# Kernel optimization log

Hardware: AMD Instinct MI355X
Metric: run time of the kernel (lower is better)

Reference implementation:

```python
import jax, jax.numpy as jnp
import numpy as np

B, N = 8, 1000
EMB, K, F1E, F1V, MSG = 4, 3, 2, 3, 2


def cross_concat(h):
    # h: [b, n, d] -> [b, n, n, 2d], interleaving (h_i, h_j) per feature (stack axis=-1 then reshape)
    b, n, d = h.shape
    hi = jnp.broadcast_to(h[:, :, None, :], (b, n, n, d))
    hj = jnp.broadcast_to(h[:, None, :, :], (b, n, n, d))
    return jnp.stack((hi, hj), axis=-1).reshape(b, n, n, 2 * d)


def setup_inputs() -> dict:
    key = jax.random.key(0)
    ks = jax.random.split(key, 16)
    p = lambda k, s: (jax.random.normal(k, s, dtype=jnp.float32) * 0.1)
    return {
        "x": jax.random.normal(ks[0], (B, N), dtype=jnp.float32),
        "W1_emb": p(ks[1], (1, EMB)), "b1_emb": p(ks[2], (EMB,)),
        "W2_emb": p(ks[3], (1, EMB)), "b2_emb": p(ks[4], (EMB,)),
        "W_f1e": p(ks[5], (2 * EMB, F1E)), "b_f1e": p(ks[6], (F1E,)),
        "W_f2e": p(ks[7], (2 * F1V, K)), "b_f2e": p(ks[8], (K,)),
        "W_fk": p(ks[9], (K, 2 * EMB, MSG)), "b_fk": p(ks[10], (K, MSG)),
        "W_f1v": p(ks[11], (F1E, F1V)), "b_f1v": p(ks[12], (F1V,)),
        "W_f2v": p(ks[13], (MSG + 1, 1)), "b_f2v": p(ks[14], (1,)),
    }


def reference(x, W1_emb, b1_emb, W2_emb, b2_emb, W_f1e, b_f1e, W_f2e, b_f2e,
              W_fk, b_fk, W_f1v, b_f1v, W_f2v, b_f2v):
    x_ = x[..., None]                                  # [B,N,1]
    h1 = x_ @ W1_emb + b1_emb                          # [B,N,EMB]
    c = cross_concat(h1)                               # [B,N,N,2*EMB]
    h = jnp.sum(c @ W_f1e + b_f1e, axis=2)             # [B,N,F1E]
    h2 = h @ W_f1v + b_f1v                             # [B,N,F1V]
    c2 = cross_concat(h2)                              # [B,N,N,2*F1V]
    hsum = jnp.sum(c2, axis=0)                         # [N,N,2*F1V] (sum over batch)
    edge_logits = hsum @ W_f2e + b_f2e                 # [N,N,K]
    edge_probs = jax.nn.softmax(edge_logits, axis=-1)  # [N,N,K]
    h1_ = x_ @ W2_emb + b2_emb                         # [B,N,EMB]
    c3 = cross_concat(h1_)                             # [B,N,N,2*EMB]
    # K per-relation edge MLPs, stacked on the last axis -> [B,N,N,MSG,K]
    messages = jnp.einsum('bijd,kdm->bijmk', c3, W_fk) + b_fk.T
    # softmax-weighted combine, summed over receiver axis j and relation axis k
    v_e = jnp.einsum('ijk,bijmk->bim', edge_probs, messages)  # [B,N,MSG]
    h2_ = x_ + (jnp.concatenate((v_e, x_), axis=-1) @ W_f2v + b_f2v)
    return jnp.squeeze(h2_, axis=-1)                   # [B,N]
```

## Files before the change

kernel.cpp:

```cpp
#include <hip/hip_runtime.h>

#define NN 1000

__device__ __forceinline__ float wave_sum(float v) {
#pragma unroll
    for (int o = 32; o > 0; o >>= 1) v += __shfl_xor(v, o, 64);
    return v;
}

__global__ __launch_bounds__(256) void fused_kernel(
    const float* __restrict__ x,
    const float* __restrict__ W1, const float* __restrict__ b1,
    const float* __restrict__ W2, const float* __restrict__ b2,
    const float* __restrict__ Wf1e, const float* __restrict__ bf1e,
    const float* __restrict__ Wf2e, const float* __restrict__ bf2e,
    const float* __restrict__ Wfk, const float* __restrict__ bfk,
    const float* __restrict__ Wf1v, const float* __restrict__ bf1v,
    const float* __restrict__ Wf2v, const float* __restrict__ bf2v,
    float* __restrict__ out) {
    const int wave = threadIdx.x >> 6;
    const int lane = threadIdx.x & 63;
    const int i = blockIdx.x * 4 + wave;

    float4 v[4][8];
#pragma unroll
    for (int t = 0; t < 4; ++t) {
        const int j4 = lane + 64 * t;
        if (j4 < NN / 4) {
#pragma unroll
            for (int b = 0; b < 8; ++b)
                v[t][b] = *reinterpret_cast<const float4*>(x + b * NN + 4 * j4);
        }
    }

    float Xs[8];
#pragma unroll
    for (int b = 0; b < 8; ++b) {
        float sb = 0.f;
#pragma unroll
        for (int t = 0; t < 4; ++t)
            if (lane + 64 * t < NN / 4)
                sb += (v[t][b].x + v[t][b].y) + (v[t][b].z + v[t][b].w);
        Xs[b] = wave_sum(sb);
    }
    const float S = ((Xs[0] + Xs[1]) + (Xs[2] + Xs[3])) +
                    ((Xs[4] + Xs[5]) + (Xs[6] + Xs[7]));

    float alpha[2];
#pragma unroll
    for (int f = 0; f < 2; ++f) {
        float a = 0.f;
#pragma unroll
        for (int e = 0; e < 4; ++e) a += W1[e] * Wf1e[(2 * e) * 2 + f];
        alpha[f] = (float)NN * a;
    }
    float gamma[3];
#pragma unroll
    for (int vv = 0; vv < 3; ++vv) {
        float g = 0.f;
#pragma unroll
        for (int f = 0; f < 2; ++f) g += alpha[f] * Wf1v[f * 3 + vv];
        gamma[vv] = g;
    }
    float uA[6], cB[6], vAc[6];
#pragma unroll
    for (int m = 0; m < 2; ++m)
#pragma unroll
        for (int k = 0; k < 3; ++k) {
            float ua = 0.f, ub = 0.f, va = 0.f, vb = 0.f;
#pragma unroll
            for (int e = 0; e < 4; ++e) {
                float wE = Wfk[k * 16 + (2 * e) * 2 + m];
                float wO = Wfk[k * 16 + (2 * e + 1) * 2 + m];
                ua += W2[e] * wE; ub += b2[e] * wE;
                va += W2[e] * wO; vb += b2[e] * wO;
            }
            uA[m * 3 + k]  = ua;
            cB[m * 3 + k]  = ub + vb + bfk[k * 2 + m];
            vAc[m * 3 + k] = va;
        }
    float Bsum[2];
#pragma unroll
    for (int f = 0; f < 2; ++f) {
        float t0 = 0.f, t1 = 0.f;
#pragma unroll
        for (int e = 0; e < 4; ++e) {
            t0 += b1[e] * Wf1e[(2 * e) * 2 + f];
            t1 += (S * W1[e] + 8.f * (float)NN * b1[e]) * Wf1e[(2 * e + 1) * 2 + f];
        }
        Bsum[f] = 8.f * (float)NN * t0 + t1 + 8.f * (float)NN * bf1e[f];
    }
    float Ds[3];
#pragma unroll
    for (int vv = 0; vv < 3; ++vv) {
        float d = 8.f * bf1v[vv];
#pragma unroll
        for (int f = 0; f < 2; ++f) d += Bsum[f] * Wf1v[f * 3 + vv];
        Ds[vv] = d;
    }
    const float LOG2E = 1.4426950408889634f;
    float PB[3], AiQ[3];
    {
        float xsi = 0.f;
#pragma unroll
        for (int b = 0; b < 8; ++b) xsi += x[b * NN + i];
#pragma unroll
        for (int k = 0; k < 3; ++k) {
            float PA = 0.f, QA = 0.f, pb = 0.f, qb = 0.f;
#pragma unroll
            for (int vv = 0; vv < 3; ++vv) {
                PA += gamma[vv] * Wf2e[(2 * vv) * 3 + k];
                QA += Ds[vv]    * Wf2e[(2 * vv) * 3 + k];
                pb += gamma[vv] * Wf2e[(2 * vv + 1) * 3 + k];
                qb += Ds[vv]    * Wf2e[(2 * vv + 1) * 3 + k];
            }
            PB[k]  = pb * LOG2E;
            AiQ[k] = (PA * xsi + QA + bf2e[k] + qb) * LOG2E;
        }
    }

    const float ai0 = AiQ[0], ai1 = AiQ[1], ai2 = AiQ[2];
    const float pb0 = PB[0], pb1 = PB[1], pb2 = PB[2];
    float Q0 = 0.f, Q1 = 0.f;
    float R[8][2];
#pragma unroll
    for (int b = 0; b < 8; ++b) { R[b][0] = 0.f; R[b][1] = 0.f; }

#pragma unroll
    for (int t = 0; t < 4; ++t) {
        if (lane + 64 * t < NN / 4) {
            const float* vf = reinterpret_cast<const float*>(v[t]);
#pragma unroll
            for (int u = 0; u < 4; ++u) {
                float xs = 0.f;
#pragma unroll
                for (int b = 0; b < 8; ++b) xs += vf[b * 4 + u];
                float l0 = ai0 + pb0 * xs, l1 = ai1 + pb1 * xs, l2 = ai2 + pb2 * xs;
                float mx = fmaxf(l0, fmaxf(l1, l2));
                float e0 = exp2f(l0 - mx), e1 = exp2f(l1 - mx), e2 = exp2f(l2 - mx);
                float inv = 1.f / (e0 + e1 + e2);
                float p0 = e0 * inv, p1 = e1 * inv;
                Q0 += p0; Q1 += p1;
#pragma unroll
                for (int b = 0; b < 8; ++b) {
                    float xb = vf[b * 4 + u];
                    R[b][0] += p0 * xb;
                    R[b][1] += p1 * xb;
                }
            }
        }
    }

    Q0 = wave_sum(Q0); Q1 = wave_sum(Q1);
#pragma unroll
    for (int b = 0; b < 8; ++b) {
        R[b][0] = wave_sum(R[b][0]);
        R[b][1] = wave_sum(R[b][1]);
    }

    if (lane < 8) {
        const int b = lane;
        float xi = x[b * NN + i];
        float Q2 = (float)NN - Q0 - Q1;
        float Rk0 = R[b][0], Rk1 = R[b][1];
        float Rk2 = Xs[b] - Rk0 - Rk1;
        float ve[2];
#pragma unroll
        for (int m = 0; m < 2; ++m) {
            ve[m] = Q0 * (uA[m * 3 + 0] * xi + cB[m * 3 + 0]) + vAc[m * 3 + 0] * Rk0
                  + Q1 * (uA[m * 3 + 1] * xi + cB[m * 3 + 1]) + vAc[m * 3 + 1] * Rk1
                  + Q2 * (uA[m * 3 + 2] * xi + cB[m * 3 + 2]) + vAc[m * 3 + 2] * Rk2;
        }
        out[b * NN + i] = xi + ve[0] * Wf2v[0] + ve[1] * Wf2v[1] + xi * Wf2v[2] + bf2v[0];
    }
}

extern "C" void kernel_launch(void* const* d_in, const int* in_sizes, int n_in,
                              void* d_out, int out_size, void* d_ws, size_t ws_size,
                              hipStream_t stream) {
    const float* x    = (const float*)d_in[0];
    const float* W1   = (const float*)d_in[1];
    const float* b1   = (const float*)d_in[2];
    const float* W2   = (const float*)d_in[3];
    const float* b2   = (const float*)d_in[4];
    const float* Wf1e = (const float*)d_in[5];
    const float* bf1e = (const float*)d_in[6];
    const float* Wf2e = (const float*)d_in[7];
    const float* bf2e = (const float*)d_in[8];
    const float* Wfk  = (const float*)d_in[9];
    const float* bfk  = (const float*)d_in[10];
    const float* Wf1v = (const float*)d_in[11];
    const float* bf1v = (const float*)d_in[12];
    const float* Wf2v = (const float*)d_in[13];
    const float* bf2v = (const float*)d_in[14];

    fused_kernel<<<NN / 4, 256, 0, stream>>>(x, W1, b1, W2, b2, Wf1e, bf1e,
                                             Wf2e, bf2e, Wfk, bfk, Wf1v, bf1v,
                                             Wf2v, bf2v, (float*)d_out);
}
```

Measured before the change: 90.87 us.

## Assign one block per output row instead of one wave per row

Each block now handles a single row i, spreading the 250 float4 columns across 256 threads instead of one wave looping over four chunks. Partial sums are reduced across waves through shared memory with two barriers. The grid grows from 250 to 1000 blocks, which raises parallelism and cuts per-thread register use and serial work. The cost is block-level synchronization, and every block still rereads the whole x array.

```diff
diff --git a/kernel.cpp b/kernel.cpp
--- a/kernel.cpp
+++ b/kernel.cpp
@@ -18,33 +18,34 @@
     const float* __restrict__ Wf1v, const float* __restrict__ bf1v,
     const float* __restrict__ Wf2v, const float* __restrict__ bf2v,
     float* __restrict__ out) {
-    const int wave = threadIdx.x >> 6;
-    const int lane = threadIdx.x & 63;
-    const int i = blockIdx.x * 4 + wave;
-
-    float4 v[4][8];
-#pragma unroll
-    for (int t = 0; t < 4; ++t) {
-        const int j4 = lane + 64 * t;
-        if (j4 < NN / 4) {
-#pragma unroll
-            for (int b = 0; b < 8; ++b)
-                v[t][b] = *reinterpret_cast<const float4*>(x + b * NN + 4 * j4);
-        }
-    }
-
-    float Xs[8];
+    const int tid  = threadIdx.x;
+    const int wave = tid >> 6;
+    const int lane = tid & 63;
+    const int i    = blockIdx.x;
+    const bool act = tid < (NN / 4);
+
+    __shared__ float redA[4][8];
+    __shared__ float redB[4][18];
+
+    float4 v[8];
+#pragma unroll
+    for (int b = 0; b < 8; ++b)
+        v[b] = act ? *reinterpret_cast<const float4*>(x + b * NN + 4 * tid)
+                   : make_float4(0.f, 0.f, 0.f, 0.f);
+    float xsi = 0.f;
+#pragma unroll
+    for (int b = 0; b < 8; ++b) xsi += x[b * NN + i];
+
+    float part[8];
 #pragma unroll
     for (int b = 0; b < 8; ++b) {
-        float sb = 0.f;
-#pragma unroll
-        for (int t = 0; t < 4; ++t)
-            if (lane + 64 * t < NN / 4)
-                sb += (v[t][b].x + v[t][b].y) + (v[t][b].z + v[t][b].w);
-        Xs[b] = wave_sum(sb);
-    }
-    const float S = ((Xs[0] + Xs[1]) + (Xs[2] + Xs[3])) +
-                    ((Xs[4] + Xs[5]) + (Xs[6] + Xs[7]));
+        float s = (v[b].x + v[b].y) + (v[b].z + v[b].w);
+        part[b] = wave_sum(s);
+    }
+    if (lane == 0) {
+#pragma unroll
+        for (int b = 0; b < 8; ++b) redA[wave][b] = part[b];
+    }
 
     float alpha[2];
 #pragma unroll
@@ -79,6 +80,28 @@
             cB[m * 3 + k]  = ub + vb + bfk[k * 2 + m];
             vAc[m * 3 + k] = va;
         }
+    const float LOG2E = 1.4426950408889634f;
+    float PA[3], PB[3], pbv[3];
+#pragma unroll
+    for (int k = 0; k < 3; ++k) {
+        float pa = 0.f, pb = 0.f;
+#pragma unroll
+        for (int vv = 0; vv < 3; ++vv) {
+            pa += gamma[vv] * Wf2e[(2 * vv) * 3 + k];
+            pb += gamma[vv] * Wf2e[(2 * vv + 1) * 3 + k];
+        }
+        PA[k] = pa; pbv[k] = pb;
+        PB[k] = pb * LOG2E;
+    }
+
+    __syncthreads();
+
+    float Xs[8];
+#pragma unroll
+    for (int b = 0; b < 8; ++b)
+        Xs[b] = (redA[0][b] + redA[1][b]) + (redA[2][b] + redA[3][b]);
+    const float S = ((Xs[0] + Xs[1]) + (Xs[2] + Xs[3])) +
+                    ((Xs[4] + Xs[5]) + (Xs[6] + Xs[7]));
     float Bsum[2];
 #pragma unroll
     for (int f = 0; f < 2; ++f) {
@@ -98,25 +121,16 @@
         for (int f = 0; f < 2; ++f) d += Bsum[f] * Wf1v[f * 3 + vv];
         Ds[vv] = d;
     }
-    const float LOG2E = 1.4426950408889634f;
-    float PB[3], AiQ[3];
-    {
-        float xsi = 0.f;
-#pragma unroll
-        for (int b = 0; b < 8; ++b) xsi += x[b * NN + i];
-#pragma unroll
-        for (int k = 0; k < 3; ++k) {
-            float PA = 0.f, QA = 0.f, pb = 0.f, qb = 0.f;
-#pragma unroll
-            for (int vv = 0; vv < 3; ++vv) {
-                PA += gamma[vv] * Wf2e[(2 * vv) * 3 + k];
-                QA += Ds[vv]    * Wf2e[(2 * vv) * 3 + k];
-                pb += gamma[vv] * Wf2e[(2 * vv + 1) * 3 + k];
-                qb += Ds[vv]    * Wf2e[(2 * vv + 1) * 3 + k];
-            }
-            PB[k]  = pb * LOG2E;
-            AiQ[k] = (PA * xsi + QA + bf2e[k] + qb) * LOG2E;
-        }
+    float AiQ[3];
+#pragma unroll
+    for (int k = 0; k < 3; ++k) {
+        float QA = 0.f, qb = 0.f;
+#pragma unroll
+        for (int vv = 0; vv < 3; ++vv) {
+            QA += Ds[vv] * Wf2e[(2 * vv) * 3 + k];
+            qb += Ds[vv] * Wf2e[(2 * vv + 1) * 3 + k];
+        }
+        AiQ[k] = (PA[k] * xsi + QA + bf2e[k] + qb) * LOG2E;
     }
 
     const float ai0 = AiQ[0], ai1 = AiQ[1], ai2 = AiQ[2];
@@ -126,27 +140,24 @@
 #pragma unroll
     for (int b = 0; b < 8; ++b) { R[b][0] = 0.f; R[b][1] = 0.f; }
 
-#pragma unroll
-    for (int t = 0; t < 4; ++t) {
-        if (lane + 64 * t < NN / 4) {
-            const float* vf = reinterpret_cast<const float*>(v[t]);
-#pragma unroll
-            for (int u = 0; u < 4; ++u) {
-                float xs = 0.f;
-#pragma unroll
-                for (int b = 0; b < 8; ++b) xs += vf[b * 4 + u];
-                float l0 = ai0 + pb0 * xs, l1 = ai1 + pb1 * xs, l2 = ai2 + pb2 * xs;
-                float mx = fmaxf(l0, fmaxf(l1, l2));
-                float e0 = exp2f(l0 - mx), e1 = exp2f(l1 - mx), e2 = exp2f(l2 - mx);
-                float inv = 1.f / (e0 + e1 + e2);
-                float p0 = e0 * inv, p1 = e1 * inv;
-                Q0 += p0; Q1 += p1;
-#pragma unroll
-                for (int b = 0; b < 8; ++b) {
-                    float xb = vf[b * 4 + u];
-                    R[b][0] += p0 * xb;
-                    R[b][1] += p1 * xb;
-                }
+    if (act) {
+        const float* vf = reinterpret_cast<const float*>(v);
+#pragma unroll
+        for (int u = 0; u < 4; ++u) {
+            float xs = 0.f;
+#pragma unroll
+            for (int b = 0; b < 8; ++b) xs += vf[b * 4 + u];
+            float l0 = ai0 + pb0 * xs, l1 = ai1 + pb1 * xs, l2 = ai2 + pb2 * xs;
+            float mx = fmaxf(l0, fmaxf(l1, l2));
+            float e0 = exp2f(l0 - mx), e1 = exp2f(l1 - mx), e2 = exp2f(l2 - mx);
+            float inv = 1.f / (e0 + e1 + e2);
+            float p0 = e0 * inv, p1 = e1 * inv;
+            Q0 += p0; Q1 += p1;
+#pragma unroll
+            for (int b = 0; b < 8; ++b) {
+                float xb = vf[b * 4 + u];
+                R[b][0] += p0 * xb;
+                R[b][1] += p1 * xb;
             }
         }
     }
@@ -157,18 +168,32 @@
         R[b][0] = wave_sum(R[b][0]);
         R[b][1] = wave_sum(R[b][1]);
     }
-
-    if (lane < 8) {
-        const int b = lane;
-        float xi = x[b * NN + i];
-        float Q2 = (float)NN - Q0 - Q1;
-        float Rk0 = R[b][0], Rk1 = R[b][1];
+    if (lane == 0) {
+        redB[wave][0] = Q0; redB[wave][1] = Q1;
+#pragma unroll
+        for (int b = 0; b < 8; ++b) {
+            redB[wave][2 + 2 * b] = R[b][0];
+            redB[wave][3 + 2 * b] = R[b][1];
+        }
+    }
+    __syncthreads();
+
+    if (tid < 8) {
+        const int b = tid;
+        float q0  = (redB[0][0] + redB[1][0]) + (redB[2][0] + redB[3][0]);
+        float q1  = (redB[0][1] + redB[1][1]) + (redB[2][1] + redB[3][1]);
+        float Rk0 = (redB[0][2 + 2 * b] + redB[1][2 + 2 * b]) +
+                    (redB[2][2 + 2 * b] + redB[3][2 + 2 * b]);
+        float Rk1 = (redB[0][3 + 2 * b] + redB[1][3 + 2 * b]) +
+                    (redB[2][3 + 2 * b] + redB[3][3 + 2 * b]);
+        float xi  = x[b * NN + i];
+        float Q2  = (float)NN - q0 - q1;
         float Rk2 = Xs[b] - Rk0 - Rk1;
         float ve[2];
 #pragma unroll
         for (int m = 0; m < 2; ++m) {
-            ve[m] = Q0 * (uA[m * 3 + 0] * xi + cB[m * 3 + 0]) + vAc[m * 3 + 0] * Rk0
-                  + Q1 * (uA[m * 3 + 1] * xi + cB[m * 3 + 1]) + vAc[m * 3 + 1] * Rk1
+            ve[m] = q0 * (uA[m * 3 + 0] * xi + cB[m * 3 + 0]) + vAc[m * 3 + 0] * Rk0
+                  + q1 * (uA[m * 3 + 1] * xi + cB[m * 3 + 1]) + vAc[m * 3 + 1] * Rk1
                   + Q2 * (uA[m * 3 + 2] * xi + cB[m * 3 + 2]) + vAc[m * 3 + 2] * Rk2;
         }
         out[b * NN + i] = xi + ve[0] * Wf2v[0] + ve[1] * Wf2v[1] + xi * Wf2v[2] + bf2v[0];
@@ -194,7 +219,7 @@
     const float* Wf2v = (const float*)d_in[13];
     const float* bf2v = (const float*)d_in[14];
 
-    fused_kernel<<<NN / 4, 256, 0, stream>>>(x, W1, b1, W2, b2, Wf1e, bf1e,
-                                             Wf2e, bf2e, Wfk, bfk, Wf1v, bf1v,
-                                             Wf2v, bf2v, (float*)d_out);
+    fused_kernel<<<NN, 256, 0, stream>>>(x, W1, b1, W2, b2, Wf1e, bf1e,
+                                         Wf2e, bf2e, Wfk, bfk, Wf1v, bf1v,
+                                         Wf2v, bf2v, (float*)d_out);
 }
```

Result: slower. 93.82 us (+3.2%).
